# Optimization experiments

Hardware: AMD Instinct MI355X
Metric: run time of the kernel (lower is better)

## Reference

```python
import jax, jax.numpy as jnp
import numpy as np

B, L, S, D, H, M, DFF, CO = 16, 512, 1024, 512, 8, 64, 2048, 512
KS = (3, 5, 7)  # MOEDecomp kernel sizes


def _avgpool(x, k):
    # AvgPool1d(kernel=k, stride=1, padding=k//2, count_include_pad=True) along L of [B,L,D]
    p = k // 2
    s = jax.lax.reduce_window(x, 0.0, jax.lax.add, (1, k, 1), (1, 1, 1), ((0, 0), (p, p), (0, 0)))
    return s / k


def _moe_decomp(x, w1, b1, w2, b2):
    trends = jnp.stack([_avgpool(x, k) for k in KS], axis=-1)          # [B,L,D,E]
    g = jax.nn.softmax(jax.nn.relu(x @ w1.T + b1) @ w2.T + b2, axis=-1)  # [B,L,E]
    trend = jnp.einsum('blde,ble->bld', trends, g)
    return x - trend, trend


def _fourier_block(x, wr, wi):
    b, l, d = x.shape
    qft = jnp.fft.rfft(x, axis=1)                                      # [B, L//2+1, D] complex
    m = min(M, qft.shape[1])
    W = wr[:, :, :m] + 1j * wi[:, :, :m]                               # [D,D,m] complex
    om = jnp.einsum('bmd,dem->bme', qft[:, :m], W)                     # per-mode complex matmul
    out_ft = jnp.zeros((b, l // 2 + 1, d), jnp.complex64).at[:, :m].set(om)
    return jnp.fft.irfft(out_ft, n=l, axis=1)


def _fourier_cross(q_in, kv, wq, bq, wk, bk, wv, bv, wo, bo):
    b, l, _ = q_in.shape
    s = kv.shape[1]
    dk = D // H
    q = (q_in @ wq.T + bq).reshape(b, l, H, dk).transpose(0, 2, 1, 3)   # [B,H,L,dk]
    k = (kv @ wk.T + bk).reshape(b, s, H, dk).transpose(0, 2, 1, 3)
    v = (kv @ wv.T + bv).reshape(b, s, H, dk).transpose(0, 2, 1, 3)
    qf = jnp.fft.rfft(q, axis=2)
    kf = jnp.fft.rfft(k, axis=2)
    vf = jnp.fft.rfft(v, axis=2)
    mq = min(M, qf.shape[2])
    mk = min(M, kf.shape[2])
    qf, kf, vf = qf[:, :, :mq], kf[:, :, :mk], vf[:, :, :mk]
    attn = (jnp.einsum('bhld,bhsd->bhls', qf.real, kf.real)
            + jnp.einsum('bhld,bhsd->bhls', qf.imag, kf.imag))
    attn = jax.nn.softmax(attn, axis=-1)
    of = jax.lax.complex(jnp.einsum('bhls,bhsd->bhld', attn, vf.real),
                         jnp.einsum('bhls,bhsd->bhld', attn, vf.imag))
    full = jnp.zeros((b, H, l // 2 + 1, dk), jnp.complex64).at[:, :, :mq].set(of)
    out = jnp.fft.irfft(full, n=l, axis=2)                              # [B,H,L,dk]
    out = out.transpose(0, 2, 1, 3).reshape(b, l, D)
    return out @ wo.T + bo


def _circ_conv(t, w):
    # Conv1d(k=3, padding=1, circular, no bias); t: [B,L,D], w: [CO,D,3]
    xt = t.transpose(0, 2, 1)                                           # [B,D,L]
    xp = jnp.concatenate([xt[:, :, -1:], xt, xt[:, :, :1]], axis=-1)
    y = jax.lax.conv_general_dilated(xp, w, (1,), 'VALID',
                                     dimension_numbers=('NCH', 'OIH', 'NCH'))
    return y.transpose(0, 2, 1)                                         # [B,L,CO]


def setup_inputs() -> dict:
    key = jax.random.key(0)
    ks = jax.random.split(key, 32)
    def n(i, shape, scale=0.02):
        return (scale * jax.random.normal(ks[i], shape)).astype(jnp.float32)
    feb_scale = 1.0 / (D * D)
    inp = {
        'x': n(0, (B, L, D), 1.0),
        'cross': n(1, (B, S, D), 1.0),
        'feb_wr': n(2, (D, D, M), feb_scale),
        'feb_wi': n(3, (D, D, M), feb_scale),
        'wq': n(4, (D, D)), 'bq': n(5, (D,)),
        'wk': n(6, (D, D)), 'bk': n(7, (D,)),
        'wv': n(8, (D, D)), 'bv': n(9, (D,)),
        'wo': n(10, (D, D)), 'bo': n(11, (D,)),
        'w_ff1': n(12, (DFF, D)), 'w_ff2': n(13, (D, DFF)),
        'd1_w1': n(14, (D // 2, D)), 'd1_b1': n(15, (D // 2,)),
        'd1_w2': n(16, (3, D // 2)), 'd1_b2': n(17, (3,)),
        'd2_w1': n(18, (D // 2, D)), 'd2_b1': n(19, (D // 2,)),
        'd2_w2': n(20, (3, D // 2)), 'd2_b2': n(21, (3,)),
        'd3_w1': n(22, (D // 2, D)), 'd3_b1': n(23, (D // 2,)),
        'd3_w2': n(24, (3, D // 2)), 'd3_b2': n(25, (3,)),
        'p1': n(26, (CO, D, 3)), 'p2': n(27, (CO, D, 3)), 'p3': n(28, (CO, D, 3)),
    }
    return inp


def reference(x, cross, feb_wr, feb_wi, wq, bq, wk, bk, wv, bv, wo, bo,
              w_ff1, w_ff2, d1_w1, d1_b1, d1_w2, d1_b2,
              d2_w1, d2_b1, d2_w2, d2_b2, d3_w1, d3_b1, d3_w2, d3_b2,
              p1, p2, p3):
    # dropout is identity (eval mode)
    x = x + _fourier_block(x, feb_wr, feb_wi)
    x, t1 = _moe_decomp(x, d1_w1, d1_b1, d1_w2, d1_b2)
    x = x + _fourier_cross(x, cross, wq, bq, wk, bk, wv, bv, wo, bo)
    x, t2 = _moe_decomp(x, d2_w1, d2_b1, d2_w2, d2_b2)
    y = jax.nn.relu(x @ w_ff1.T) @ w_ff2.T  # 1x1 convs == pointwise GEMMs
    x, t3 = _moe_decomp(x + y, d3_w1, d3_b1, d3_w2, d3_b2)
    residual_trend = _circ_conv(t1, p1) + _circ_conv(t2, p2) + _circ_conv(t3, p3)
    return x, residual_trend
```

## Files before the change

### kernel.cpp

```cpp
#include <hip/hip_runtime.h>
#include <math.h>

typedef unsigned short u16;
typedef unsigned int u32;
typedef unsigned long long u64;

constexpr int kB = 16, kL = 512, kS = 1024, kD = 512, kM = 64;

typedef __attribute__((ext_vector_type(8))) short u16x8;
typedef __attribute__((ext_vector_type(8))) _Float16 f16x8;
typedef __attribute__((ext_vector_type(4))) float f32x4;

__device__ __forceinline__ u16 f2h(float f) {
    _Float16 h = (_Float16)f;
    return *(u16*)&h;
}
__device__ __forceinline__ float h2f(u16 u) {
    _Float16 h = *(_Float16*)&u;
    return (float)h;
}

__global__ __launch_bounds__(256, 4) void gemm_fp16(
    const u16* __restrict__ Abase, const u16* __restrict__ Wbase,
    const float* __restrict__ bias, const float* __restrict__ resid,
    float* __restrict__ Cout, u16* __restrict__ Ch,
    int R, int N, int K, int flags,
    u64 zsA, u64 zsW, u64 zsC, u64 zsR, int lrsh)
{
    __shared__ __attribute__((aligned(16))) u16 Abuf[128 * 64];
    __shared__ __attribute__((aligned(16))) u16 Bbuf[128 * 64];
    const int zz = blockIdx.z;
    Abase += (u64)zz * zsA;
    Wbase += (u64)zz * zsW;
    if (Cout) Cout += (u64)zz * zsC;
    if (Ch)   Ch   += (u64)zz * zsC;
    if (resid) resid += (u64)zz * zsR;

    const int tid = threadIdx.x;
    const int lane = tid & 63;
    const int wave = tid >> 6;
    const int wr = wave >> 1, wc = wave & 1;
    const int ln15 = lane & 15, lq = lane >> 4;
    const int r0 = blockIdx.y * 128, n0 = blockIdx.x * 128;

    f32x4 acc[4][4];
#pragma unroll
    for (int m = 0; m < 4; ++m)
#pragma unroll
        for (int n = 0; n < 4; ++n) acc[m][n] = (f32x4){0.f, 0.f, 0.f, 0.f};

    for (int k0 = 0; k0 < K; k0 += 64) {
        u16x8 av[4], bv[4];
#pragma unroll
        for (int it = 0; it < 4; ++it) {
            int c = it * 256 + tid;
            int row = c >> 3, j = c & 7;
            int jj = j ^ (row & 7);
            av[it] = *(const u16x8*)(Abase + (size_t)(r0 + row) * K + k0 + jj * 8);
            bv[it] = *(const u16x8*)(Wbase + (size_t)(n0 + row) * K + k0 + jj * 8);
        }
        __syncthreads();
#pragma unroll
        for (int it = 0; it < 4; ++it) {
            int c = it * 256 + tid;
            int row = c >> 3, j = c & 7;
            *(u16x8*)&Abuf[row * 64 + j * 8] = av[it];
            *(u16x8*)&Bbuf[row * 64 + j * 8] = bv[it];
        }
        __syncthreads();
#pragma unroll
        for (int h = 0; h < 2; ++h) {
            int kg = lq + h * 4;
            f16x8 af[4], bfv[4];
#pragma unroll
            for (int m = 0; m < 4; ++m) {
                int row = wr * 64 + m * 16 + ln15;
                af[m] = *(const f16x8*)&Abuf[row * 64 + ((kg ^ (row & 7)) << 3)];
            }
#pragma unroll
            for (int n = 0; n < 4; ++n) {
                int col = wc * 64 + n * 16 + ln15;
                bfv[n] = *(const f16x8*)&Bbuf[col * 64 + ((kg ^ (col & 7)) << 3)];
            }
#pragma unroll
            for (int m = 0; m < 4; ++m)
#pragma unroll
                for (int n = 0; n < 4; ++n)
                    acc[m][n] = __builtin_amdgcn_mfma_f32_16x16x32_f16(af[m], bfv[n], acc[m][n], 0, 0, 0);
        }
        __syncthreads();
    }

#pragma unroll
    for (int m = 0; m < 4; ++m) {
#pragma unroll
        for (int n = 0; n < 4; ++n) {
            int gc = n0 + wc * 64 + n * 16 + ln15;
            float bv_ = bias ? bias[gc] : 0.f;
            int gr0 = r0 + wr * 64 + m * 16 + lq * 4;
            float v[4];
#pragma unroll
            for (int rg = 0; rg < 4; ++rg) {
                int gr = gr0 + rg;
                float val = acc[m][n][rg] + bv_;
                if (resid) val += resid[(size_t)gr * N + gc];
                if (flags & 1) val = fmaxf(val, 0.f);
                if (flags & 16) Cout[(size_t)gr * N + gc] = val;
                if (flags & 8)  Ch[(size_t)gr * N + gc] = f2h(val);
                v[rg] = val;
            }
            if (flags & 32) {
                int bb = gr0 >> lrsh;
                int l_ = gr0 & ((1 << lrsh) - 1);
                ushort4 o;
                o.x = f2h(v[0]); o.y = f2h(v[1]); o.z = f2h(v[2]); o.w = f2h(v[3]);
                *(ushort4*)&Ch[(((size_t)bb * N + gc) << lrsh) + l_] = o;
            }
        }
    }
}

__global__ __launch_bounds__(256, 4) void gemm64(
    const u16* __restrict__ Abase, const u16* __restrict__ Wbase,
    const float* __restrict__ bias, const float* __restrict__ resid,
    float* __restrict__ Cout, u16* __restrict__ Ch,
    int R, int N, int K, int flags,
    u64 zsA, u64 zsW, u64 zsC, u64 zsR)
{
    __shared__ __attribute__((aligned(16))) u16 Abuf[64 * 64];
    __shared__ __attribute__((aligned(16))) u16 Bbuf[64 * 64];
    const int zz = blockIdx.z;
    Abase += (u64)zz * zsA;
    Wbase += (u64)zz * zsW;
    if (Cout) Cout += (u64)zz * zsC;
    if (Ch)   Ch   += (u64)zz * zsC;
    if (resid) resid += (u64)zz * zsR;

    const int tid = threadIdx.x;
    const int lane = tid & 63;
    const int w = tid >> 6;
    const int ln15 = lane & 15, lq = lane >> 4;
    const int r0 = blockIdx.y * 64, n0 = blockIdx.x * 64;

    f32x4 acc[4];
#pragma unroll
    for (int m = 0; m < 4; ++m) acc[m] = (f32x4){0.f, 0.f, 0.f, 0.f};

    for (int k0 = 0; k0 < K; k0 += 64) {
        u16x8 av[2], bv[2];
#pragma unroll
        for (int it = 0; it < 2; ++it) {
            int c = it * 256 + tid;
            int row = c >> 3, j = c & 7;
            int jj = j ^ (row & 7);
            av[it] = *(const u16x8*)(Abase + (size_t)(r0 + row) * K + k0 + jj * 8);
            bv[it] = *(const u16x8*)(Wbase + (size_t)(n0 + row) * K + k0 + jj * 8);
        }
        __syncthreads();
#pragma unroll
        for (int it = 0; it < 2; ++it) {
            int c = it * 256 + tid;
            int row = c >> 3, j = c & 7;
            *(u16x8*)&Abuf[row * 64 + j * 8] = av[it];
            *(u16x8*)&Bbuf[row * 64 + j * 8] = bv[it];
        }
        __syncthreads();
#pragma unroll
        for (int h = 0; h < 2; ++h) {
            int kg = lq + h * 4;
            int col = w * 16 + ln15;
            f16x8 bf = *(const f16x8*)&Bbuf[col * 64 + ((kg ^ (col & 7)) << 3)];
#pragma unroll
            for (int m = 0; m < 4; ++m) {
                int row = m * 16 + ln15;
                f16x8 af = *(const f16x8*)&Abuf[row * 64 + ((kg ^ (row & 7)) << 3)];
                acc[m] = __builtin_amdgcn_mfma_f32_16x16x32_f16(af, bf, acc[m], 0, 0, 0);
            }
        }
        __syncthreads();
    }

    const int gc = n0 + w * 16 + ln15;
    const float bv_ = bias ? bias[gc] : 0.f;
#pragma unroll
    for (int m = 0; m < 4; ++m) {
        int gr0 = r0 + m * 16 + lq * 4;
#pragma unroll
        for (int rg = 0; rg < 4; ++rg) {
            int gr = gr0 + rg;
            float val = acc[m][rg] + bv_;
            if (resid) val += resid[(size_t)gr * N + gc];
            if (flags & 1) val = fmaxf(val, 0.f);
            if (flags & 16) Cout[(size_t)gr * N + gc] = val;
            if (flags & 8)  Ch[(size_t)gr * N + gc] = f2h(val);
        }
    }
}

__global__ __launch_bounds__(256) void prep(
    const float* __restrict__ wq, const float* __restrict__ wk,
    const float* __restrict__ wv, const float* __restrict__ wo,
    const float* __restrict__ ff1, const float* __restrict__ ff2,
    const float* __restrict__ dw1, const float* __restrict__ dw2,
    const float* __restrict__ dw3, const float* __restrict__ cross,
    const float* __restrict__ bk, const float* __restrict__ bv,
    u16* __restrict__ wqh, u16* __restrict__ wkvh, u16* __restrict__ woh,
    u16* __restrict__ ff1h, u16* __restrict__ ff2h,
    u16* __restrict__ d1w1h, u16* __restrict__ d2w1h, u16* __restrict__ d3w1h,
    u16* __restrict__ crossh, float* __restrict__ bkv,
    u16* __restrict__ tw512, u16* __restrict__ tw1024, u16* __restrict__ tih)
{
    const int gid = blockIdx.x * 256 + threadIdx.x;
    const int stride = gridDim.x * 256;
    for (int i = gid; i < 262144; i += stride) wqh[i] = f2h(wq[i]);
    for (int i = gid; i < 262144; i += stride) wkvh[i] = f2h(wk[i]);
    for (int i = gid; i < 262144; i += stride) wkvh[262144 + i] = f2h(wv[i]);
    for (int i = gid; i < 262144; i += stride) woh[i] = f2h(wo[i]);
    for (int i = gid; i < 1048576; i += stride) ff1h[i] = f2h(ff1[i]);
    for (int i = gid; i < 1048576; i += stride) ff2h[i] = f2h(ff2[i]);
    for (int i = gid; i < 131072; i += stride) d1w1h[i] = f2h(dw1[i]);
    for (int i = gid; i < 131072; i += stride) d2w1h[i] = f2h(dw2[i]);
    for (int i = gid; i < 131072; i += stride) d3w1h[i] = f2h(dw3[i]);
    const float4* c4 = (const float4*)cross;
    for (int i = gid; i < 2097152; i += stride) {
        float4 v = c4[i];
        ushort4 o;
        o.x = f2h(v.x); o.y = f2h(v.y); o.z = f2h(v.z); o.w = f2h(v.w);
        *(ushort4*)&crossh[i * 4] = o;
    }
    for (int i = gid; i < 1024; i += stride) bkv[i] = (i < 512) ? bk[i] : bv[i - 512];
    for (int i = gid; i < 65536; i += stride) {
        int r = i >> 9, l = i & 511;
        int m = r & 63;
        int ph = (m * l) & 511;
        float ang = 6.283185307179586f * (float)ph / 512.0f;
        float s_, c_;
        sincosf(ang, &s_, &c_);
        tw512[i] = f2h((r < 64) ? c_ : -s_);
    }
    for (int i = gid; i < 131072; i += stride) {
        int r = i >> 10, l = i & 1023;
        int m = r & 63;
        int ph = (m * l) & 1023;
        float ang = 6.283185307179586f * (float)ph / 1024.0f;
        float s_, c_;
        sincosf(ang, &s_, &c_);
        tw1024[i] = f2h((r < 64) ? c_ : -s_);
    }
    for (int i = gid; i < 65536; i += stride) {
        int l = i >> 7, r = i & 127;
        int m = r & 63;
        int ph = (m * l) & 511;
        float ang = 6.283185307179586f * (float)ph / 512.0f;
        float s_, c_;
        sincosf(ang, &s_, &c_);
        float val;
        if (r == 0) val = 1.0f / 512.0f;
        else if (r < 64) val = 2.0f * c_ / 512.0f;
        else if (r == 64) val = 0.0f;
        else val = -2.0f * s_ / 512.0f;
        tih[i] = f2h(val);
    }
}

__global__ __launch_bounds__(256) void tr_cast_x(
    const float* __restrict__ x, u16* __restrict__ xt)
{
    __shared__ u16 t[64][72];
    const int b = blockIdx.y;
    const int lt = (blockIdx.x >> 3) * 64, dt = (blockIdx.x & 7) * 64;
    const int tid = threadIdx.x;
#pragma unroll
    for (int rep = 0; rep < 16; ++rep) {
        int idx = tid + rep * 256;
        int row = idx >> 6, col = idx & 63;
        t[row][col] = f2h(x[((size_t)b * kL + lt + row) * kD + dt + col]);
    }
    __syncthreads();
#pragma unroll
    for (int rep = 0; rep < 16; ++rep) {
        int idx = tid + rep * 256;
        int row = idx >> 6, col = idx & 63;
        xt[((size_t)b * kD + dt + row) * kL + lt + col] = t[col][row];
    }
}

__global__ __launch_bounds__(256) void spec_tr(
    const float* __restrict__ QF, float* __restrict__ qtr, float* __restrict__ qti)
{
    __shared__ float t0[64][65], t1[64][65];
    const int b = blockIdx.y;
    const int dt = blockIdx.x * 64;
    const int tid = threadIdx.x;
    const float* QFb = QF + (size_t)b * 128 * 512;
#pragma unroll
    for (int rep = 0; rep < 16; ++rep) {
        int idx = tid + rep * 256;
        int m = idx >> 6, dd = idx & 63;
        t0[m][dd] = QFb[(size_t)m * 512 + dt + dd];
        t1[m][dd] = QFb[(size_t)(64 + m) * 512 + dt + dd];
    }
    __syncthreads();
#pragma unroll
    for (int rep = 0; rep < 16; ++rep) {
        int idx = tid + rep * 256;
        int dd = idx >> 6, m = idx & 63;
        size_t o = ((size_t)(dt + dd) * kB + b) * kM + m;
        qtr[o] = t0[m][dd];
        qti[o] = t1[m][dd];
    }
}

__global__ __launch_bounds__(256) void feb_part(
    const float* __restrict__ qtr, const float* __restrict__ qti,
    const float* __restrict__ wr, const float* __restrict__ wi,
    float* __restrict__ part)
{
    __shared__ float sqr[4][16][64], sqi[4][16][64];
    const int eb = blockIdx.x;
    const int ch = blockIdx.y;
    const int tid = threadIdx.x;
    const int mm = tid & 63, ee = tid >> 6;
    const int e = eb * 4 + ee;
    float ar[16], ai[16];
#pragma unroll
    for (int b_ = 0; b_ < 16; ++b_) { ar[b_] = 0.f; ai[b_] = 0.f; }

    const int dbeg = ch * 128, dend = dbeg + 128;
    for (int d0 = dbeg; d0 < dend; d0 += 4) {
        __syncthreads();
#pragma unroll
        for (int rep = 0; rep < 16; ++rep) {
            int idx = tid + rep * 256;
            int m_ = idx & 63, b_ = (idx >> 6) & 15, dd_ = idx >> 10;
            size_t g = ((size_t)(d0 + dd_) * kB + b_) * kM + m_;
            sqr[dd_][b_][m_] = qtr[g];
            sqi[dd_][b_][m_] = qti[g];
        }
        __syncthreads();
#pragma unroll
        for (int dd = 0; dd < 4; ++dd) {
            size_t wofs = ((size_t)(d0 + dd) * kD + e) * kM + mm;
            float wrv = wr[wofs], wiv = wi[wofs];
#pragma unroll
            for (int b_ = 0; b_ < 16; ++b_) {
                float qr = sqr[dd][b_][mm], qi = sqi[dd][b_][mm];
                ar[b_] += qr * wrv - qi * wiv;
                ai[b_] += qr * wiv + qi * wrv;
            }
        }
    }
    float* reg = part + (size_t)(ch * 128 + eb) * 8192;
#pragma unroll
    for (int b_ = 0; b_ < 16; ++b_) {
        reg[(b_ * 64 + mm) * 4 + ee] = ar[b_];
        reg[4096 + (b_ * 64 + mm) * 4 + ee] = ai[b_];
    }
}

__global__ __launch_bounds__(256) void feb_reduce(
    const float* __restrict__ part, u16* __restrict__ OMT)
{
    int idx = blockIdx.x * 256 + threadIdx.x;
    int m = idx & 63, e = (idx >> 6) & 511, b = idx >> 15;
    int eb = e >> 2, ee = e & 3;
    float r = 0.f, im = 0.f;
#pragma unroll
    for (int ch = 0; ch < 4; ++ch) {
        const float* reg = part + (size_t)(ch * 128 + eb) * 8192 + ((b * 64 + m) * 4 + ee);
        r += reg[0];
        im += reg[4096];
    }
    u16* o = OMT + ((size_t)(b * 512 + e)) * 128;
    o[m] = f2h(r);
    o[64 + m] = f2h(im);
}

__global__ __launch_bounds__(256) void spectral_attn(
    const float* __restrict__ QF, const float* __restrict__ KVF,
    u16* __restrict__ OMT)
{
    __shared__ float kr[64][65], ki[64][65], sat[64][65];
    const int b = blockIdx.x >> 3, h = blockIdx.x & 7;
    const int tid = threadIdx.x;
    const int dbase = h * 64;
    const float* KVFb = KVF + (size_t)b * 128 * 1024;

    for (int idx = tid; idx < 4096; idx += 256) {
        int j = idx >> 6, dd = idx & 63;
        kr[j][dd] = KVFb[(size_t)j * 1024 + dbase + dd];
        ki[j][dd] = KVFb[(size_t)(64 + j) * 1024 + dbase + dd];
    }
    __syncthreads();

    const int i_ = tid >> 2, jg = tid & 3;
    float s[16];
#pragma unroll
    for (int jj = 0; jj < 16; ++jj) s[jj] = 0.f;
    const float* qrp = QF + ((size_t)b * 128 + i_) * 512 + dbase;
    const float* qip = qrp + (size_t)64 * 512;
    for (int dd = 0; dd < 64; ++dd) {
        float qr = qrp[dd], qi = qip[dd];
#pragma unroll
        for (int jj = 0; jj < 16; ++jj) {
            int j = jg * 16 + jj;
            s[jj] += qr * kr[j][dd] + qi * ki[j][dd];
        }
    }
    float mx = s[0];
#pragma unroll
    for (int jj = 1; jj < 16; ++jj) mx = fmaxf(mx, s[jj]);
    mx = fmaxf(mx, __shfl_xor(mx, 1));
    mx = fmaxf(mx, __shfl_xor(mx, 2));
    float sum = 0.f;
#pragma unroll
    for (int jj = 0; jj < 16; ++jj) { s[jj] = expf(s[jj] - mx); sum += s[jj]; }
    sum += __shfl_xor(sum, 1);
    sum += __shfl_xor(sum, 2);
    float rinv = 1.0f / sum;
#pragma unroll
    for (int jj = 0; jj < 16; ++jj) sat[i_][jg * 16 + jj] = s[jj] * rinv;
    __syncthreads();

    const int dd = tid & 63, ig = tid >> 6;
    float ar[16], ai[16];
#pragma unroll
    for (int ii = 0; ii < 16; ++ii) { ar[ii] = 0.f; ai[ii] = 0.f; }
    const float* VFb = KVFb + 512 + dbase + dd;
    for (int j = 0; j < 64; ++j) {
        float vr = VFb[(size_t)j * 1024];
        float vi = VFb[(size_t)(64 + j) * 1024];
#pragma unroll
        for (int ii = 0; ii < 16; ++ii) {
            float a = sat[ig * 16 + ii][j];
            ar[ii] += a * vr;
            ai[ii] += a * vi;
        }
    }
    u16* o = OMT + ((size_t)(b * 512 + dbase + dd)) * 128 + ig * 16;
    u16x8 v0, v1, w0, w1;
#pragma unroll
    for (int q = 0; q < 8; ++q) {
        v0[q] = (short)f2h(ar[q]);     v1[q] = (short)f2h(ar[8 + q]);
        w0[q] = (short)f2h(ai[q]);     w1[q] = (short)f2h(ai[8 + q]);
    }
    *(u16x8*)(o) = v0;
    *(u16x8*)(o + 8) = v1;
    *(u16x8*)(o + 64) = w0;
    *(u16x8*)(o + 72) = w1;
}

__global__ __launch_bounds__(256) void decomp_apply(
    const float* __restrict__ x, const float* __restrict__ logits,
    float* __restrict__ xout, u16* __restrict__ xout_h, u16* __restrict__ tout_h)
{
    int idx = blockIdx.x * 256 + threadIdx.x;
    if (idx >= kB * kL * kD) return;
    int d = idx & 511;
    int l = (idx >> 9) & 511;
    int b = idx >> 18;
    const float* lg = logits + ((size_t)b * kL + l) * 3;
    float g0 = lg[0], g1 = lg[1], g2 = lg[2];
    float m = fmaxf(g0, fmaxf(g1, g2));
    float e0 = expf(g0 - m), e1 = expf(g1 - m), e2 = expf(g2 - m);
    float inv = 1.0f / (e0 + e1 + e2);
    g0 = e0 * inv; g1 = e1 * inv; g2 = e2 * inv;

    const float* xb = x + (size_t)b * kL * kD + d;
    float v[7];
#pragma unroll
    for (int j = 0; j < 7; ++j) {
        int ls = l + j - 3;
        v[j] = (ls >= 0 && ls < kL) ? xb[(size_t)ls * kD] : 0.f;
    }
    float s3 = (v[2] + v[3] + v[4]) * (1.0f / 3.0f);
    float s5 = (v[1] + v[2] + v[3] + v[4] + v[5]) * 0.2f;
    float s7 = (v[0] + v[1] + v[2] + v[3] + v[4] + v[5] + v[6]) * (1.0f / 7.0f);
    float trend = g0 * s3 + g1 * s5 + g2 * s7;
    float res = v[3] - trend;
    if (xout) xout[idx] = res;
    if (xout_h) xout_h[idx] = f2h(res);
    tout_h[idx] = f2h(trend);
}

__global__ __launch_bounds__(256) void gate2(
    const u16* __restrict__ GH, const float* __restrict__ w2,
    const float* __restrict__ b2, float* __restrict__ logits)
{
    __shared__ float w2l[3][256];
    int tid = threadIdx.x;
    for (int i = tid; i < 768; i += 256) w2l[i >> 8][i & 255] = w2[i];
    __syncthreads();
    int r = blockIdx.x * 256 + tid;
    float s0 = b2[0], s1 = b2[1], s2 = b2[2];
    const u16* g = GH + (size_t)r * 256;
    for (int c0 = 0; c0 < 256; c0 += 8) {
        uint4 u = *(const uint4*)&g[c0];
        u32 w[4] = {u.x, u.y, u.z, u.w};
#pragma unroll
        for (int p = 0; p < 4; ++p) {
            float f0 = h2f((u16)(w[p] & 0xFFFF));
            float f1 = h2f((u16)(w[p] >> 16));
            int c = c0 + p * 2;
            s0 += f0 * w2l[0][c] + f1 * w2l[0][c + 1];
            s1 += f0 * w2l[1][c] + f1 * w2l[1][c + 1];
            s2 += f0 * w2l[2][c] + f1 * w2l[2][c + 1];
        }
    }
    logits[(size_t)r * 3 + 0] = s0;
    logits[(size_t)r * 3 + 1] = s1;
    logits[(size_t)r * 3 + 2] = s2;
}

__global__ void repack_p(const float* __restrict__ p1, const float* __restrict__ p2,
                         const float* __restrict__ p3, u16* __restrict__ pk)
{
    int idx = blockIdx.x * 256 + threadIdx.x;
    if (idx >= 3 * 3 * 512 * 512) return;
    int d = idx & 511;
    int oc = (idx >> 9) & 511;
    int j = (idx / (512 * 512)) % 3;
    int t = idx / (3 * 512 * 512);
    const float* p = (t == 0) ? p1 : (t == 1) ? p2 : p3;
    pk[idx] = f2h(p[(size_t)oc * 512 * 3 + (size_t)d * 3 + j]);
}

__global__ __launch_bounds__(256) void conv_sum(
    const u16* __restrict__ Cc, float* __restrict__ outt)
{
    int gid = blockIdx.x * 256 + threadIdx.x;
    int ocg = gid & 63;
    int r = gid >> 6;
    int b = r >> 9, l = r & 511;
    float s[8];
#pragma unroll
    for (int q = 0; q < 8; ++q) s[q] = 0.f;
#pragma unroll
    for (int t = 0; t < 3; ++t) {
#pragma unroll
        for (int j = 0; j < 3; ++j) {
            int lr = (l + j + 511) & 511;
            const u16x8 v = *(const u16x8*)&Cc[(size_t)t * 8192 * 1536 +
                ((size_t)(b * 512 + lr)) * 1536 + j * 512 + ocg * 8];
#pragma unroll
            for (int q = 0; q < 8; ++q) s[q] += h2f((u16)v[q]);
        }
    }
    float4 o0 = {s[0], s[1], s[2], s[3]};
    float4 o1 = {s[4], s[5], s[6], s[7]};
    *(float4*)&outt[(size_t)r * 512 + ocg * 8] = o0;
    *(float4*)&outt[(size_t)r * 512 + ocg * 8 + 4] = o1;
}

extern "C" void kernel_launch(void* const* d_in, const int* in_sizes, int n_in,
                              void* d_out, int out_size, void* d_ws, size_t ws_size,
                              hipStream_t stream)
{
    const float* x_in   = (const float*)d_in[0];
    const float* cross  = (const float*)d_in[1];
    const float* feb_wr = (const float*)d_in[2];
    const float* feb_wi = (const float*)d_in[3];
    const float* wq = (const float*)d_in[4];
    const float* bq = (const float*)d_in[5];
    const float* wk = (const float*)d_in[6];
    const float* bk = (const float*)d_in[7];
    const float* wv = (const float*)d_in[8];
    const float* bv = (const float*)d_in[9];
    const float* wo = (const float*)d_in[10];
    const float* bo = (const float*)d_in[11];
    const float* w_ff1 = (const float*)d_in[12];
    const float* w_ff2 = (const float*)d_in[13];
    const float* d1_w1 = (const float*)d_in[14];
    const float* d1_b1 = (const float*)d_in[15];
    const float* d1_w2 = (const float*)d_in[16];
    const float* d1_b2 = (const float*)d_in[17];
    const float* d2_w1 = (const float*)d_in[18];
    const float* d2_b1 = (const float*)d_in[19];
    const float* d2_w2 = (const float*)d_in[20];
    const float* d2_b2 = (const float*)d_in[21];
    const float* d3_w1 = (const float*)d_in[22];
    const float* d3_b1 = (const float*)d_in[23];
    const float* d3_w2 = (const float*)d_in[24];
    const float* d3_b2 = (const float*)d_in[25];
    const float* p1 = (const float*)d_in[26];
    const float* p2 = (const float*)d_in[27];
    const float* p3 = (const float*)d_in[28];

    float* ws = (float*)d_ws;
    float* X    = ws;
    float* XT   = ws + 4194304;
    u16*  KVt   = (u16*)(ws + 8388608);
    u16*  Q0t   = (u16*)(ws + 16777216);
    u16*  T1h   = (u16*)(ws + 18874368);
    u16*  T2h   = (u16*)(ws + 20971520);
    u16*  T3h   = (u16*)(ws + 23068672);
    float* QF   = ws + 25165824;
    float* KVF  = ws + 26214400;
    u16*  OMTh  = (u16*)(ws + 28311552);
    float* QTr  = ws + 28835840;
    float* QTi  = ws + 29360128;
    u16*  crossh = (u16*)(ws + 29884416);
    u16*  Xh    = (u16*)(ws + 34078720);
    u16*  XTh   = (u16*)(ws + 36175872);
    u16*  GHh   = (u16*)(ws + 38273024);
    float* GLG  = ws + 39321600;
    u16*  wqh   = (u16*)(ws + 39346176);
    u16*  wkvh  = wqh + 262144;
    u16*  woh   = wkvh + 524288;
    u16*  ff1h  = woh + 262144;
    u16*  ff2h  = ff1h + 1048576;
    u16*  d1w1h = ff2h + 1048576;
    u16*  d2w1h = d1w1h + 131072;
    u16*  d3w1h = d2w1h + 131072;
    u16*  PKh   = d3w1h + 131072;
    u16*  TW512h  = (u16*)(ws + 42295296);
    u16*  TW1024h = (u16*)(ws + 42328064);
    u16*  TIh     = (u16*)(ws + 42393600);
    float* bkv    = ws + 42426368;
    float* FEBP = (float*)KVt;
    u16*  xTh   = (u16*)(ws + 12582912);
    u16*  HIDh  = KVt;
    u16*  Qh    = Q0t;
    u16*  Cch   = (u16*)ws;

    float* outx = (float*)d_out;
    float* outt = outx + 4194304;

    auto g128 = [&](const u16* A, const u16* W, const float* bias, const float* resid,
                    float* C, u16* Cb, int R, int N, int K, int flags,
                    int Z, u64 zsA, u64 zsW, u64 zsC, u64 zsR, int lrsh) {
        dim3 g(N / 128, R / 128, Z);
        hipLaunchKernelGGL(gemm_fp16, g, dim3(256), 0, stream,
                           A, W, bias, resid, C, Cb, R, N, K, flags, zsA, zsW, zsC, zsR, lrsh);
    };
    auto g64 = [&](const u16* A, const u16* W, const float* bias, const float* resid,
                   float* C, u16* Cb, int R, int N, int K, int flags,
                   int Z, u64 zsA, u64 zsW, u64 zsC, u64 zsR) {
        dim3 g(N / 64, R / 64, Z);
        hipLaunchKernelGGL(gemm64, g, dim3(256), 0, stream,
                           A, W, bias, resid, C, Cb, R, N, K, flags, zsA, zsW, zsC, zsR);
    };

    hipLaunchKernelGGL(prep, dim3(2048), dim3(256), 0, stream,
                       wq, wk, wv, wo, w_ff1, w_ff2, d1_w1, d2_w1, d3_w1, cross, bk, bv,
                       wqh, wkvh, woh, ff1h, ff2h, d1w1h, d2w1h, d3w1h, crossh, bkv,
                       TW512h, TW1024h, TIh);
    hipLaunchKernelGGL(repack_p, dim3(9216), dim3(256), 0, stream, p1, p2, p3, PKh);

    hipLaunchKernelGGL(tr_cast_x, dim3(64, 16), dim3(256), 0, stream, x_in, xTh);
    g64(TW512h, xTh, nullptr, nullptr, QF, nullptr, 128, 512, 512, 16,
        16, 0, (u64)512 * 512, (u64)128 * 512, 0);
    hipLaunchKernelGGL(spec_tr, dim3(8, 16), dim3(256), 0, stream, QF, QTr, QTi);
    hipLaunchKernelGGL(feb_part, dim3(128, 4), dim3(256), 0, stream, QTr, QTi, feb_wr, feb_wi, FEBP);
    hipLaunchKernelGGL(feb_reduce, dim3(2048), dim3(256), 0, stream, FEBP, OMTh);
    g64(TIh, OMTh, nullptr, x_in, X, Xh, 512, 512, 128, 16 | 8,
        16, 0, (u64)512 * 128, (u64)512 * 512, (u64)512 * 512);

    g64(Xh, d1w1h, d1_b1, nullptr, nullptr, GHh, 8192, 256, 512, 1 | 8, 1, 0, 0, 0, 0);
    hipLaunchKernelGGL(gate2, dim3(32), dim3(256), 0, stream, GHh, d1_w2, d1_b2, GLG);
    hipLaunchKernelGGL(decomp_apply, dim3(16384), dim3(256), 0, stream, X, GLG, XT, XTh, T1h);

    g128(XTh, wqh, bq, nullptr, nullptr, Q0t, 8192, 512, 512, 32, 1, 0, 0, 0, 0, 9);
    g128(crossh, wkvh, bkv, nullptr, nullptr, KVt, 16384, 1024, 512, 32, 1, 0, 0, 0, 0, 10);
    g64(TW512h, Q0t, nullptr, nullptr, QF, nullptr, 128, 512, 512, 16,
        16, 0, (u64)512 * 512, (u64)128 * 512, 0);
    g64(TW1024h, KVt, nullptr, nullptr, KVF, nullptr, 128, 1024, 1024, 16,
        16, 0, (u64)1024 * 1024, (u64)128 * 1024, 0);
    hipLaunchKernelGGL(spectral_attn, dim3(128), dim3(256), 0, stream, QF, KVF, OMTh);
    g64(TIh, OMTh, nullptr, nullptr, nullptr, Qh, 512, 512, 128, 8,
        16, 0, (u64)512 * 128, (u64)512 * 512, 0);
    g128(Qh, woh, bo, XT, X, Xh, 8192, 512, 512, 16 | 8, 1, 0, 0, 0, 0, 0);

    g64(Xh, d2w1h, d2_b1, nullptr, nullptr, GHh, 8192, 256, 512, 1 | 8, 1, 0, 0, 0, 0);
    hipLaunchKernelGGL(gate2, dim3(32), dim3(256), 0, stream, GHh, d2_w2, d2_b2, GLG);
    hipLaunchKernelGGL(decomp_apply, dim3(16384), dim3(256), 0, stream, X, GLG, XT, XTh, T2h);

    g128(XTh, ff1h, nullptr, nullptr, nullptr, HIDh, 8192, 2048, 512, 1 | 8, 1, 0, 0, 0, 0, 0);
    g128(HIDh, ff2h, nullptr, XT, X, Xh, 8192, 512, 2048, 16 | 8, 1, 0, 0, 0, 0, 0);

    g64(Xh, d3w1h, d3_b1, nullptr, nullptr, GHh, 8192, 256, 512, 1 | 8, 1, 0, 0, 0, 0);
    hipLaunchKernelGGL(gate2, dim3(32), dim3(256), 0, stream, GHh, d3_w2, d3_b2, GLG);
    hipLaunchKernelGGL(decomp_apply, dim3(16384), dim3(256), 0, stream, X, GLG, outx,
                       (u16*)nullptr, T3h);

    g128(T1h, PKh, nullptr, nullptr, nullptr, Cch, 8192, 1536, 512, 8,
         3, (u64)8192 * 512, (u64)1536 * 512, (u64)8192 * 1536, 0, 0);
    hipLaunchKernelGGL(conv_sum, dim3(2048), dim3(256), 0, stream, Cch, outt);

    (void)in_sizes; (void)n_in; (void)out_size; (void)ws_size;
}
```

Before: 596.4 us.

## Rebalance FEB partial matmul, parallelize gate logits, move small GEMMs to 64-tile kernel

```diff
diff --git a/kernel.cpp b/kernel.cpp
--- a/kernel.cpp
+++ b/kernel.cpp
@@ -125,7 +125,7 @@
     const float* __restrict__ bias, const float* __restrict__ resid,
     float* __restrict__ Cout, u16* __restrict__ Ch,
     int R, int N, int K, int flags,
-    u64 zsA, u64 zsW, u64 zsC, u64 zsR)
+    u64 zsA, u64 zsW, u64 zsC, u64 zsR, int lrsh)
 {
     __shared__ __attribute__((aligned(16))) u16 Abuf[64 * 64];
     __shared__ __attribute__((aligned(16))) u16 Bbuf[64 * 64];
@@ -185,6 +185,7 @@
 #pragma unroll
     for (int m = 0; m < 4; ++m) {
         int gr0 = r0 + m * 16 + lq * 4;
+        float v[4];
 #pragma unroll
         for (int rg = 0; rg < 4; ++rg) {
             int gr = gr0 + rg;
@@ -193,6 +194,14 @@
             if (flags & 1) val = fmaxf(val, 0.f);
             if (flags & 16) Cout[(size_t)gr * N + gc] = val;
             if (flags & 8)  Ch[(size_t)gr * N + gc] = f2h(val);
+            v[rg] = val;
+        }
+        if (flags & 32) {
+            int bb = gr0 >> lrsh;
+            int l_ = gr0 & ((1 << lrsh) - 1);
+            ushort4 o;
+            o.x = f2h(v[0]); o.y = f2h(v[1]); o.z = f2h(v[2]); o.w = f2h(v[3]);
+            *(ushort4*)&Ch[(((size_t)bb * N + gc) << lrsh) + l_] = o;
         }
     }
 }
@@ -311,65 +320,66 @@
     }
 }
 
-__global__ __launch_bounds__(256) void feb_part(
+__global__ __launch_bounds__(256, 2) void feb_part2(
     const float* __restrict__ qtr, const float* __restrict__ qti,
     const float* __restrict__ wr, const float* __restrict__ wi,
-    float* __restrict__ part)
+    float2* __restrict__ part)
 {
     __shared__ float sqr[4][16][64], sqi[4][16][64];
-    const int eb = blockIdx.x;
-    const int ch = blockIdx.y;
+    const int eb = blockIdx.x, ch = blockIdx.y;
     const int tid = threadIdx.x;
-    const int mm = tid & 63, ee = tid >> 6;
-    const int e = eb * 4 + ee;
-    float ar[16], ai[16];
-#pragma unroll
-    for (int b_ = 0; b_ < 16; ++b_) { ar[b_] = 0.f; ai[b_] = 0.f; }
-
-    const int dbeg = ch * 128, dend = dbeg + 128;
+    const int mm = tid & 63, eq = tid >> 6;
+    const int e0 = eb * 8 + eq * 2;
+
+    float ar0[16], ai0[16], ar1[16], ai1[16];
+#pragma unroll
+    for (int b = 0; b < 16; ++b) { ar0[b] = 0.f; ai0[b] = 0.f; ar1[b] = 0.f; ai1[b] = 0.f; }
+
+    const int dbeg = ch * 64, dend = dbeg + 64;
     for (int d0 = dbeg; d0 < dend; d0 += 4) {
         __syncthreads();
 #pragma unroll
         for (int rep = 0; rep < 16; ++rep) {
             int idx = tid + rep * 256;
             int m_ = idx & 63, b_ = (idx >> 6) & 15, dd_ = idx >> 10;
-            size_t g = ((size_t)(d0 + dd_) * kB + b_) * kM + m_;
+            size_t g = (size_t)(d0 + dd_) * 1024 + b_ * 64 + m_;
             sqr[dd_][b_][m_] = qtr[g];
             sqi[dd_][b_][m_] = qti[g];
         }
         __syncthreads();
 #pragma unroll
         for (int dd = 0; dd < 4; ++dd) {
-            size_t wofs = ((size_t)(d0 + dd) * kD + e) * kM + mm;
-            float wrv = wr[wofs], wiv = wi[wofs];
-#pragma unroll
-            for (int b_ = 0; b_ < 16; ++b_) {
-                float qr = sqr[dd][b_][mm], qi = sqi[dd][b_][mm];
-                ar[b_] += qr * wrv - qi * wiv;
-                ai[b_] += qr * wiv + qi * wrv;
+            size_t w0 = ((size_t)(d0 + dd) * 512 + e0) * 64 + mm;
+            float wr0 = wr[w0],      wi0 = wi[w0];
+            float wr1 = wr[w0 + 64], wi1 = wi[w0 + 64];
+#pragma unroll
+            for (int b = 0; b < 16; ++b) {
+                float qr = sqr[dd][b][mm], qi = sqi[dd][b][mm];
+                ar0[b] += qr * wr0 - qi * wi0;
+                ai0[b] += qr * wi0 + qi * wr0;
+                ar1[b] += qr * wr1 - qi * wi1;
+                ai1[b] += qr * wi1 + qi * wr1;
             }
         }
     }
-    float* reg = part + (size_t)(ch * 128 + eb) * 8192;
-#pragma unroll
-    for (int b_ = 0; b_ < 16; ++b_) {
-        reg[(b_ * 64 + mm) * 4 + ee] = ar[b_];
-        reg[4096 + (b_ * 64 + mm) * 4 + ee] = ai[b_];
+#pragma unroll
+    for (int b = 0; b < 16; ++b) {
+        part[((size_t)(ch * 512 + e0) * 16 + b) * 64 + mm]       = make_float2(ar0[b], ai0[b]);
+        part[((size_t)(ch * 512 + e0 + 1) * 16 + b) * 64 + mm]   = make_float2(ar1[b], ai1[b]);
     }
 }
 
 __global__ __launch_bounds__(256) void feb_reduce(
-    const float* __restrict__ part, u16* __restrict__ OMT)
+    const float2* __restrict__ part, u16* __restrict__ OMT)
 {
     int idx = blockIdx.x * 256 + threadIdx.x;
     int m = idx & 63, e = (idx >> 6) & 511, b = idx >> 15;
-    int eb = e >> 2, ee = e & 3;
     float r = 0.f, im = 0.f;
 #pragma unroll
-    for (int ch = 0; ch < 4; ++ch) {
-        const float* reg = part + (size_t)(ch * 128 + eb) * 8192 + ((b * 64 + m) * 4 + ee);
-        r += reg[0];
-        im += reg[4096];
+    for (int ch = 0; ch < 8; ++ch) {
+        float2 v = part[((size_t)(ch * 512 + e) * 16 + b) * 64 + m];
+        r += v.x;
+        im += v.y;
     }
     u16* o = OMT + ((size_t)(b * 512 + e)) * 128;
     o[m] = f2h(r);
@@ -491,25 +501,31 @@
     int tid = threadIdx.x;
     for (int i = tid; i < 768; i += 256) w2l[i >> 8][i & 255] = w2[i];
     __syncthreads();
-    int r = blockIdx.x * 256 + tid;
-    float s0 = b2[0], s1 = b2[1], s2 = b2[2];
-    const u16* g = GH + (size_t)r * 256;
-    for (int c0 = 0; c0 < 256; c0 += 8) {
+    int gid = blockIdx.x * 256 + tid;
+    int r = gid >> 2, q = gid & 3;
+    float s0 = 0.f, s1 = 0.f, s2 = 0.f;
+    const u16* g = GH + (size_t)r * 256 + q * 64;
+    for (int c0 = 0; c0 < 64; c0 += 8) {
         uint4 u = *(const uint4*)&g[c0];
         u32 w[4] = {u.x, u.y, u.z, u.w};
 #pragma unroll
         for (int p = 0; p < 4; ++p) {
             float f0 = h2f((u16)(w[p] & 0xFFFF));
             float f1 = h2f((u16)(w[p] >> 16));
-            int c = c0 + p * 2;
+            int c = q * 64 + c0 + p * 2;
             s0 += f0 * w2l[0][c] + f1 * w2l[0][c + 1];
             s1 += f0 * w2l[1][c] + f1 * w2l[1][c + 1];
             s2 += f0 * w2l[2][c] + f1 * w2l[2][c + 1];
         }
     }
-    logits[(size_t)r * 3 + 0] = s0;
-    logits[(size_t)r * 3 + 1] = s1;
-    logits[(size_t)r * 3 + 2] = s2;
+    s0 += __shfl_xor(s0, 1); s0 += __shfl_xor(s0, 2);
+    s1 += __shfl_xor(s1, 1); s1 += __shfl_xor(s1, 2);
+    s2 += __shfl_xor(s2, 1); s2 += __shfl_xor(s2, 2);
+    if (q == 0) {
+        logits[(size_t)r * 3 + 0] = s0 + b2[0];
+        logits[(size_t)r * 3 + 1] = s1 + b2[1];
+        logits[(size_t)r * 3 + 2] = s2 + b2[2];
+    }
 }
 
 __global__ void repack_p(const float* __restrict__ p1, const float* __restrict__ p2,
@@ -617,11 +633,12 @@
     u16*  TW1024h = (u16*)(ws + 42328064);
     u16*  TIh     = (u16*)(ws + 42393600);
     float* bkv    = ws + 42426368;
-    float* FEBP = (float*)KVt;
+    float2* FEBP = (float2*)KVt;
     u16*  xTh   = (u16*)(ws + 12582912);
     u16*  HIDh  = KVt;
     u16*  Qh    = Q0t;
     u16*  Cch   = (u16*)ws;
+    xTh = Q0t;
 
     float* outx = (float*)d_out;
     float* outt = outx + 4194304;
@@ -635,10 +652,10 @@
     };
     auto g64 = [&](const u16* A, const u16* W, const float* bias, const float* resid,
                    float* C, u16* Cb, int R, int N, int K, int flags,
-                   int Z, u64 zsA, u64 zsW, u64 zsC, u64 zsR) {
+                   int Z, u64 zsA, u64 zsW, u64 zsC, u64 zsR, int lrsh) {
         dim3 g(N / 64, R / 64, Z);
         hipLaunchKernelGGL(gemm64, g, dim3(256), 0, stream,
-                           A, W, bias, resid, C, Cb, R, N, K, flags, zsA, zsW, zsC, zsR);
+                           A, W, bias, resid, C, Cb, R, N, K, flags, zsA, zsW, zsC, zsR, lrsh);
     };
 
     hipLaunchKernelGGL(prep, dim3(2048), dim3(256), 0, stream,
@@ -649,37 +666,38 @@
 
     hipLaunchKernelGGL(tr_cast_x, dim3(64, 16), dim3(256), 0, stream, x_in, xTh);
     g64(TW512h, xTh, nullptr, nullptr, QF, nullptr, 128, 512, 512, 16,
-        16, 0, (u64)512 * 512, (u64)128 * 512, 0);
+        16, 0, (u64)512 * 512, (u64)128 * 512, 0, 0);
     hipLaunchKernelGGL(spec_tr, dim3(8, 16), dim3(256), 0, stream, QF, QTr, QTi);
-    hipLaunchKernelGGL(feb_part, dim3(128, 4), dim3(256), 0, stream, QTr, QTi, feb_wr, feb_wi, FEBP);
+    hipLaunchKernelGGL(feb_part2, dim3(64, 8), dim3(256), 0, stream,
+                       QTr, QTi, feb_wr, feb_wi, FEBP);
     hipLaunchKernelGGL(feb_reduce, dim3(2048), dim3(256), 0, stream, FEBP, OMTh);
     g64(TIh, OMTh, nullptr, x_in, X, Xh, 512, 512, 128, 16 | 8,
-        16, 0, (u64)512 * 128, (u64)512 * 512, (u64)512 * 512);
-
-    g64(Xh, d1w1h, d1_b1, nullptr, nullptr, GHh, 8192, 256, 512, 1 | 8, 1, 0, 0, 0, 0);
-    hipLaunchKernelGGL(gate2, dim3(32), dim3(256), 0, stream, GHh, d1_w2, d1_b2, GLG);
+        16, 0, (u64)512 * 128, (u64)512 * 512, (u64)512 * 512, 0);
+
+    g64(Xh, d1w1h, d1_b1, nullptr, nullptr, GHh, 8192, 256, 512, 1 | 8, 1, 0, 0, 0, 0, 0);
+    hipLaunchKernelGGL(gate2, dim3(128), dim3(256), 0, stream, GHh, d1_w2, d1_b2, GLG);
     hipLaunchKernelGGL(decomp_apply, dim3(16384), dim3(256), 0, stream, X, GLG, XT, XTh, T1h);
 
-    g128(XTh, wqh, bq, nullptr, nullptr, Q0t, 8192, 512, 512, 32, 1, 0, 0, 0, 0, 9);
+    g64(XTh, wqh, bq, nullptr, nullptr, Q0t, 8192, 512, 512, 32, 1, 0, 0, 0, 0, 9);
     g128(crossh, wkvh, bkv, nullptr, nullptr, KVt, 16384, 1024, 512, 32, 1, 0, 0, 0, 0, 10);
     g64(TW512h, Q0t, nullptr, nullptr, QF, nullptr, 128, 512, 512, 16,
-        16, 0, (u64)512 * 512, (u64)128 * 512, 0);
+        16, 0, (u64)512 * 512, (u64)128 * 512, 0, 0);
     g64(TW1024h, KVt, nullptr, nullptr, KVF, nullptr, 128, 1024, 1024, 16,
-        16, 0, (u64)1024 * 1024, (u64)128 * 1024, 0);
+        16, 0, (u64)1024 * 1024, (u64)128 * 1024, 0, 0);
     hipLaunchKernelGGL(spectral_attn, dim3(128), dim3(256), 0, stream, QF, KVF, OMTh);
     g64(TIh, OMTh, nullptr, nullptr, nullptr, Qh, 512, 512, 128, 8,
-        16, 0, (u64)512 * 128, (u64)512 * 512, 0);
-    g128(Qh, woh, bo, XT, X, Xh, 8192, 512, 512, 16 | 8, 1, 0, 0, 0, 0, 0);
-
-    g64(Xh, d2w1h, d2_b1, nullptr, nullptr, GHh, 8192, 256, 512, 1 | 8, 1, 0, 0, 0, 0);
-    hipLaunchKernelGGL(gate2, dim3(32), dim3(256), 0, stream, GHh, d2_w2, d2_b2, GLG);
+        16, 0, (u64)512 * 128, (u64)512 * 512, 0, 0);
+    g64(Qh, woh, bo, XT, X, Xh, 8192, 512, 512, 16 | 8, 1, 0, 0, 0, 0, 0);
+
+    g64(Xh, d2w1h, d2_b1, nullptr, nullptr, GHh, 8192, 256, 512, 1 | 8, 1, 0, 0, 0, 0, 0);
+    hipLaunchKernelGGL(gate2, dim3(128), dim3(256), 0, stream, GHh, d2_w2, d2_b2, GLG);
     hipLaunchKernelGGL(decomp_apply, dim3(16384), dim3(256), 0, stream, X, GLG, XT, XTh, T2h);
 
     g128(XTh, ff1h, nullptr, nullptr, nullptr, HIDh, 8192, 2048, 512, 1 | 8, 1, 0, 0, 0, 0, 0);
     g128(HIDh, ff2h, nullptr, XT, X, Xh, 8192, 512, 2048, 16 | 8, 1, 0, 0, 0, 0, 0);
 
-    g64(Xh, d3w1h, d3_b1, nullptr, nullptr, GHh, 8192, 256, 512, 1 | 8, 1, 0, 0, 0, 0);
-    hipLaunchKernelGGL(gate2, dim3(32), dim3(256), 0, stream, GHh, d3_w2, d3_b2, GLG);
+    g64(Xh, d3w1h, d3_b1, nullptr, nullptr, GHh, 8192, 256, 512, 1 | 8, 1, 0, 0, 0, 0, 0);
+    hipLaunchKernelGGL(gate2, dim3(128), dim3(256), 0, stream, GHh, d3_w2, d3_b2, GLG);
     hipLaunchKernelGGL(decomp_apply, dim3(16384), dim3(256), 0, stream, X, GLG, outx,
                        (u16*)nullptr, T3h);
 
```

Result: slower. 642.4 us (+7.7%).
